# Performance work log

Hardware: AMD Instinct MI355X
Metric: run time of the kernel (lower is better)

Reference implementation:

```python
import jax, jax.numpy as jnp
import numpy as np

N_NODES = 100000
N_EDGES = 1200000
NODE_DIM = 128
HIDDEN = 64
N_POSTS = 50000


def setup_inputs() -> dict:
    key = jax.random.key(0)
    ks = jax.random.split(key, 10)
    s = 1.0 / np.sqrt(NODE_DIM)
    sh = 1.0 / np.sqrt(HIDDEN)
    return {
        "node_features": jax.random.normal(ks[0], (N_NODES, NODE_DIM), dtype=jnp.float32),
        "edge_index": jax.random.randint(ks[1], (2, N_EDGES), 0, N_NODES, dtype=jnp.int64) if jax.config.jax_enable_x64 else jax.random.randint(ks[1], (2, N_EDGES), 0, N_NODES, dtype=jnp.int32),
        "post_mask": jax.random.randint(ks[2], (N_POSTS,), 0, N_NODES, dtype=jnp.int32),
        "W_enc": jax.random.uniform(ks[3], (NODE_DIM, HIDDEN), jnp.float32, -s, s),
        "b_enc": jax.random.uniform(ks[4], (HIDDEN,), jnp.float32, -s, s),
        "W_conv": jax.random.uniform(ks[5], (HIDDEN, HIDDEN), jnp.float32, -sh, sh),
        "b_conv": jax.random.uniform(ks[6], (HIDDEN,), jnp.float32, -sh, sh),
        "W_out": jax.random.uniform(ks[7], (HIDDEN, 1), jnp.float32, -sh, sh),
        "b_out": jax.random.uniform(ks[8], (1,), jnp.float32, -sh, sh),
    }


def reference(node_features, edge_index, post_mask, W_enc, b_enc, W_conv, b_conv, W_out, b_out):
    # encode: relu(Linear)
    node_emb = jax.nn.relu(node_features @ W_enc + b_enc)  # [N, H]
    src, dst = edge_index[0], edge_index[1]
    # per-edge gather then scatter-add into destination nodes (segment sum)
    messages = jax.ops.segment_sum(node_emb[src], dst, num_segments=node_emb.shape[0])  # [N, H]
    node_emb = jax.nn.relu((node_emb + messages) @ W_conv + b_conv)  # [N, H]
    post_emb = node_emb[post_mask]  # [P, H]
    out = jax.nn.sigmoid((post_emb @ W_out + b_out).squeeze(-1))  # [P]
    return out
```

## Files before the change

kernel.cpp:

```cpp
#include <hip/hip_runtime.h>
#include <hip/hip_bf16.h>
#include <math.h>


#define HIDDEN 64
#define NODE_DIM 128
#define SCAN_CHUNK 1024

typedef __attribute__((ext_vector_type(8))) short short8;
typedef __attribute__((ext_vector_type(4))) float floatx4;

union F2B { short8 s; __hip_bfloat162 h[4]; };
union B2U { __hip_bfloat16 b; unsigned short u; };

__device__ inline short8 cvt8(const float4& p, const float4& q) {
    F2B u;
    u.h[0] = __float22bfloat162_rn(make_float2(p.x, p.y));
    u.h[1] = __float22bfloat162_rn(make_float2(p.z, p.w));
    u.h[2] = __float22bfloat162_rn(make_float2(q.x, q.y));
    u.h[3] = __float22bfloat162_rn(make_float2(q.z, q.w));
    return u.s;
}

__device__ inline void cvt8_split(const float4& p, const float4& q,
                                  short8& hi, short8& lo) {
    const float f[8] = {p.x, p.y, p.z, p.w, q.x, q.y, q.z, q.w};
    F2B uh, ul;
    #pragma unroll
    for (int jj = 0; jj < 4; ++jj) {
        const float2 v = make_float2(f[2 * jj], f[2 * jj + 1]);
        const __hip_bfloat162 h = __float22bfloat162_rn(v);
        const float2 hv = __bfloat1622float2(h);
        ul.h[jj] = __float22bfloat162_rn(make_float2(v.x - hv.x, v.y - hv.y));
        uh.h[jj] = h;
    }
    hi = uh.s; lo = ul.s;
}

__global__ __launch_bounds__(256) void k_pre(
    const int* __restrict__ post, unsigned int* __restrict__ bits,
    int* __restrict__ nodelist, int* __restrict__ listCnt,
    int* __restrict__ count, int n_posts, int n_nodes)
{
    const int gtid = blockIdx.x * 256 + threadIdx.x;
    if (gtid < n_nodes) count[gtid] = 0;
    if (gtid < n_posts) {
        const int n = post[gtid];
        const unsigned int bit = 1u << (n & 31);
        const unsigned int old = atomicOr(&bits[n >> 5], bit);
        if (!(old & bit)) {
            const int i = atomicAdd(listCnt, 1);
            nodelist[i] = n;
        }
    }
}

__global__ __launch_bounds__(256) void k_encode_count(
    const float* __restrict__ A, const float* __restrict__ We,
    const float* __restrict__ be, __hip_bfloat16* __restrict__ emb16,
    const int* __restrict__ dsts, const unsigned int* __restrict__ bits,
    int* __restrict__ count, int* __restrict__ rank,
    int n_nodes, int n_tiles, int n_edges)
{
    __shared__ unsigned short sW16[NODE_DIM * HIDDEN];

    {
        const float4* src = (const float4*)We;
        #pragma unroll
        for (int i = 0; i < 8; ++i) {
            const int fidx = i * 256 + threadIdx.x;
            const float4 v = src[fidx];
            #pragma unroll
            for (int c = 0; c < 4; ++c) {
                const int linear = fidx * 4 + c;
                const int k   = linear >> 6;
                const int col = linear & 63;
                const int ks   = k >> 5;
                const int kw   = k & 31;
                const int quad = kw >> 3;
                const int jj   = (kw & 7) >> 1;
                const int b    = kw & 1;
                const int nt   = col >> 4;
                const int r    = col & 15;
                const int dst = ((((ks * 4 + nt) * 4 + quad) * 16 + r) * 8) + jj * 2 + b;
                const float fv = (c == 0) ? v.x : (c == 1) ? v.y : (c == 2) ? v.z : v.w;
                B2U cv; cv.b = __float2bfloat16(fv);
                sW16[dst] = cv.u;
            }
        }
    }
    __syncthreads();

    const int lane = threadIdx.x & 63;
    const int r    = lane & 15;
    const int quad = lane >> 4;

    short8 Wb[4][4];
    #pragma unroll
    for (int ks = 0; ks < 4; ++ks)
        #pragma unroll
        for (int nt = 0; nt < 4; ++nt)
            Wb[ks][nt] = *(const short8*)&sW16[(((ks * 4 + nt) * 4 + quad) * 16 + r) * 8];

    float bias[4];
    #pragma unroll
    for (int nt = 0; nt < 4; ++nt) bias[nt] = be[nt * 16 + r];

    const int wid    = (blockIdx.x * 256 + threadIdx.x) >> 6;
    const int nwaves = gridDim.x * 4;

    const int estride = gridDim.x * 256;
    int e = blockIdx.x * 256 + threadIdx.x;

    for (int t = wid; t < n_tiles; t += nwaves) {
        const float* Arow = A + (size_t)t * 16 * NODE_DIM + (size_t)r * NODE_DIM + quad * 8;
        float4 a[4][2];
        #pragma unroll
        for (int ks = 0; ks < 4; ++ks) {
            a[ks][0] = *(const float4*)(Arow + ks * 32);
            a[ks][1] = *(const float4*)(Arow + ks * 32 + 4);
        }

        #pragma unroll
        for (int q = 0; q < 3; ++q) {
            if (e < n_edges) {
                const int d = dsts[e];
                if ((bits[d >> 5] >> (d & 31)) & 1u)
                    rank[e] = atomicAdd(&count[d], 1);
                e += estride;
            }
        }

        floatx4 acc[4] = {};
        #pragma unroll
        for (int ks = 0; ks < 4; ++ks) {
            const short8 af = cvt8(a[ks][0], a[ks][1]);
            #pragma unroll
            for (int nt = 0; nt < 4; ++nt)
                acc[nt] = __builtin_amdgcn_mfma_f32_16x16x32_bf16(af, Wb[ks][nt], acc[nt], 0, 0, 0);
        }
        #pragma unroll
        for (int nt = 0; nt < 4; ++nt)
            #pragma unroll
            for (int g = 0; g < 4; ++g) {
                const int node = t * 16 + quad * 4 + g;
                const float h = fmaxf(acc[nt][g] + bias[nt], 0.0f);
                emb16[(size_t)node * HIDDEN + nt * 16 + r] = __float2bfloat16(h);
            }
    }
    const int rem = n_nodes - n_tiles * 16;
    if (rem > 0 && wid == 0) {
        for (int n = n_tiles * 16; n < n_nodes; ++n) {
            float acc = be[lane];
            const float* row = A + (size_t)n * NODE_DIM;
            for (int k = 0; k < NODE_DIM; ++k)
                acc = fmaf(row[k], We[(size_t)k * HIDDEN + lane], acc);
            emb16[(size_t)n * HIDDEN + lane] = __float2bfloat16(fmaxf(acc, 0.0f));
        }
    }

    for (; e < n_edges; e += estride) {
        const int d = dsts[e];
        if ((bits[d >> 5] >> (d & 31)) & 1u)
            rank[e] = atomicAdd(&count[d], 1);
    }
}

__global__ __launch_bounds__(256) void k_scan_lb(
    const int* __restrict__ count, int* __restrict__ row_start,
    unsigned int* __restrict__ partials, int n)
{
    __shared__ int s[256];
    __shared__ int sExc;
    const int b = blockIdx.x, tid = threadIdx.x;
    const int base = b * SCAN_CHUNK + tid * 4;
    int c0 = (base + 0 < n) ? count[base + 0] : 0;
    int c1 = (base + 1 < n) ? count[base + 1] : 0;
    int c2 = (base + 2 < n) ? count[base + 2] : 0;
    int c3 = (base + 3 < n) ? count[base + 3] : 0;
    const int t = c0 + c1 + c2 + c3;
    s[tid] = t;
    __syncthreads();
    #pragma unroll
    for (int off = 1; off < 256; off <<= 1) {
        int v = (tid >= off) ? s[tid - off] : 0;
        __syncthreads();
        s[tid] += v;
        __syncthreads();
    }
    const int total = s[255];

    if (b == 0) {
        if (tid == 0) {
            __hip_atomic_store(&partials[0], (2u << 30) | (unsigned int)total,
                               __ATOMIC_RELEASE, __HIP_MEMORY_SCOPE_AGENT);
            sExc = 0;
        }
    } else {
        if (tid == 0) {
            __hip_atomic_store(&partials[b], (1u << 30) | (unsigned int)total,
                               __ATOMIC_RELEASE, __HIP_MEMORY_SCOPE_AGENT);
        }
        if (tid < 64) {
            int exc = 0;
            int winEnd = b;
            while (true) {
                const int j = winEnd - 64 + tid;
                const unsigned int v = (j >= 0)
                    ? __hip_atomic_load(&partials[j], __ATOMIC_ACQUIRE,
                                        __HIP_MEMORY_SCOPE_AGENT)
                    : (2u << 30);
                const unsigned int st = v >> 30;
                if (__ballot(st == 0u)) {
                    __builtin_amdgcn_s_sleep(1);
                    continue;
                }
                const unsigned long long b2 = __ballot(st == 2u);
                int contrib;
                bool done;
                if (b2) {
                    const int hi = 63 - __clzll(b2);
                    contrib = (tid >= hi) ? (int)(v & 0x3FFFFFFFu) : 0;
                    done = true;
                } else {
                    contrib = (int)(v & 0x3FFFFFFFu);
                    done = false;
                }
                #pragma unroll
                for (int off = 1; off < 64; off <<= 1)
                    contrib += __shfl_xor(contrib, off);
                exc += contrib;
                if (done) break;
                winEnd -= 64;
            }
            if (tid == 0) {
                __hip_atomic_store(&partials[b],
                                   (2u << 30) | (unsigned int)(exc + total),
                                   __ATOMIC_RELEASE, __HIP_MEMORY_SCOPE_AGENT);
                sExc = exc;
            }
        }
    }
    __syncthreads();
    int run = sExc + s[tid] - t;
    if (base + 0 < n) row_start[base + 0] = run;           run += c0;
    if (base + 1 < n) row_start[base + 1] = run;           run += c1;
    if (base + 2 < n) row_start[base + 2] = run;           run += c2;
    if (base + 3 < n) row_start[base + 3] = run;
}

__global__ __launch_bounds__(256) void k_fill(
    const int* __restrict__ srcs, const int* __restrict__ dsts,
    const unsigned int* __restrict__ bits, const int* __restrict__ row_start,
    const int* __restrict__ rank, int* __restrict__ slots, int n_edges)
{
    const int stride = gridDim.x * 256;
    for (int e = blockIdx.x * 256 + threadIdx.x; e < n_edges; e += stride) {
        const int d = dsts[e];
        if (!((bits[d >> 5] >> (d & 31)) & 1u)) continue;
        slots[row_start[d] + rank[e]] = srcs[e];
    }
}

__global__ __launch_bounds__(256) void k_gather(
    const int* __restrict__ nodelist, const int* __restrict__ listCnt,
    const int* __restrict__ row_start, const int* __restrict__ count,
    const int* __restrict__ slots, const __hip_bfloat16* __restrict__ emb16,
    float* __restrict__ msg_c)
{
    const int lane = threadIdx.x & 63;
    const int j    = lane & 7;
    const int g    = lane >> 3;
    const int wavei = (blockIdx.x * 256 + threadIdx.x) >> 6;
    const int ngroups = gridDim.x * 4 * 8;
    const int nc   = listCnt[0];

    for (int i = wavei * 8 + g; i < nc; i += ngroups) {
        const int n    = nodelist[i];
        const int m    = count[n];
        const int base = row_start[n];

        float2 a0 = {0.f, 0.f}, a1 = {0.f, 0.f}, a2 = {0.f, 0.f}, a3 = {0.f, 0.f};
        #define ACC8(v)  do { F2B u; u.s = (v); float2 t;                       \
            t = __bfloat1622float2(u.h[0]); a0.x += t.x; a0.y += t.y;           \
            t = __bfloat1622float2(u.h[1]); a1.x += t.x; a1.y += t.y;           \
            t = __bfloat1622float2(u.h[2]); a2.x += t.x; a2.y += t.y;           \
            t = __bfloat1622float2(u.h[3]); a3.x += t.x; a3.y += t.y; } while (0)

        {
            const short8 v = *(const short8*)(emb16 + (size_t)n * HIDDEN + j * 8);
            ACC8(v);
        }
        int c = 0;
        for (; c + 1 < m; c += 2) {
            const int s0 = slots[base + c];
            const int s1 = slots[base + c + 1];
            const short8 v0 = *(const short8*)(emb16 + (size_t)s0 * HIDDEN + j * 8);
            const short8 v1 = *(const short8*)(emb16 + (size_t)s1 * HIDDEN + j * 8);
            ACC8(v0); ACC8(v1);
        }
        if (c < m) {
            const int s0 = slots[base + c];
            const short8 v0 = *(const short8*)(emb16 + (size_t)s0 * HIDDEN + j * 8);
            ACC8(v0);
        }
        #undef ACC8

        float4* dst = (float4*)(msg_c + (size_t)i * HIDDEN + j * 8);
        dst[0] = make_float4(a0.x, a0.y, a1.x, a1.y);
        dst[1] = make_float4(a2.x, a2.y, a3.x, a3.y);
    }
}

__global__ __launch_bounds__(256) void k_head_mfma(
    const int* __restrict__ listCnt, const int* __restrict__ nodelist,
    const float* __restrict__ msg_c,
    const float* __restrict__ Wc, const float* __restrict__ bc,
    const float* __restrict__ Wo, const float* __restrict__ bo,
    float* __restrict__ res)
{
    const int lane = threadIdx.x & 63;
    const int r    = lane & 15;
    const int quad = lane >> 4;

    short8 Wb[2][4];
    #pragma unroll
    for (int ks = 0; ks < 2; ++ks)
        #pragma unroll
        for (int nt = 0; nt < 4; ++nt) {
            F2B u;
            #pragma unroll
            for (int jj = 0; jj < 4; ++jj) {
                const int k0 = ks * 32 + quad * 8 + 2 * jj;
                const float lo = Wc[(size_t)k0 * HIDDEN + nt * 16 + r];
                const float hi = Wc[(size_t)(k0 + 1) * HIDDEN + nt * 16 + r];
                u.h[jj] = __float22bfloat162_rn(make_float2(lo, hi));
            }
            Wb[ks][nt] = u.s;
        }
    float bias[4], wo[4];
    #pragma unroll
    for (int nt = 0; nt < 4; ++nt) { bias[nt] = bc[nt * 16 + r]; wo[nt] = Wo[nt * 16 + r]; }
    const float bo_s = bo[0];

    const int nc      = listCnt[0];
    const int n_tiles = (nc + 15) / 16;
    const int wid     = (blockIdx.x * 256 + threadIdx.x) >> 6;
    const int nwaves  = gridDim.x * 4;

    for (int tile = wid; tile < n_tiles; tile += nwaves) {
        const int i0  = tile * 16;
        const int row = i0 + r;
        floatx4 acc[4] = {};
        #pragma unroll
        for (int ks = 0; ks < 2; ++ks) {
            float4 f0 = make_float4(0.f, 0.f, 0.f, 0.f), f1 = f0;
            if (row < nc) {
                const float* src = msg_c + (size_t)row * HIDDEN + ks * 32 + quad * 8;
                f0 = *(const float4*)src;
                f1 = *(const float4*)(src + 4);
            }
            short8 ah, al;
            cvt8_split(f0, f1, ah, al);
            #pragma unroll
            for (int nt = 0; nt < 4; ++nt) {
                acc[nt] = __builtin_amdgcn_mfma_f32_16x16x32_bf16(ah, Wb[ks][nt], acc[nt], 0, 0, 0);
                acc[nt] = __builtin_amdgcn_mfma_f32_16x16x32_bf16(al, Wb[ks][nt], acc[nt], 0, 0, 0);
            }
        }
        float r4[4];
        #pragma unroll
        for (int gg = 0; gg < 4; ++gg) {
            float part = 0.0f;
            #pragma unroll
            for (int nt = 0; nt < 4; ++nt)
                part += fmaxf(acc[nt][gg] + bias[nt], 0.0f) * wo[nt];
            part += __shfl_xor(part, 1);
            part += __shfl_xor(part, 2);
            part += __shfl_xor(part, 4);
            part += __shfl_xor(part, 8);
            r4[gg] = part;
        }
        if (r == 0) {
            #pragma unroll
            for (int gg = 0; gg < 4; ++gg) {
                const int idx = i0 + quad * 4 + gg;
                if (idx < nc)
                    res[nodelist[idx]] = 1.0f / (1.0f + __expf(-(r4[gg] + bo_s)));
            }
        }
    }
}

__global__ __launch_bounds__(256) void k_out(
    const int* __restrict__ post, const float* __restrict__ res,
    float* __restrict__ out, int n_posts)
{
    const int p = blockIdx.x * 256 + threadIdx.x;
    if (p < n_posts) out[p] = res[post[p]];
}

extern "C" void kernel_launch(void* const* d_in, const int* in_sizes, int n_in,
                              void* d_out, int out_size, void* d_ws, size_t ws_size,
                              hipStream_t stream) {
    const float* A    = (const float*)d_in[0];
    const int*   ei   = (const int*)  d_in[1];
    const int*   post = (const int*)  d_in[2];
    const float* We   = (const float*)d_in[3];
    const float* be   = (const float*)d_in[4];
    const float* Wc   = (const float*)d_in[5];
    const float* bc   = (const float*)d_in[6];
    const float* Wo   = (const float*)d_in[7];
    const float* bo   = (const float*)d_in[8];
    float* out = (float*)d_out;

    const int n_nodes = in_sizes[0] / NODE_DIM;
    const int n_edges = in_sizes[1] / 2;
    const int n_posts = in_sizes[2];

    char* p = (char*)d_ws;
    __hip_bfloat16* emb16 = (__hip_bfloat16*)p;  p += (size_t)n_nodes * HIDDEN * 2;
    float* msg_c    = (float*)p;              p += (size_t)n_posts * HIDDEN * 4;
    int*   slots    = (int*)p;                p += (size_t)n_edges * 4;
    int*   rank     = (int*)p;                p += (size_t)n_edges * 4;
    char* zbase = p;
    unsigned int* bits = (unsigned int*)p;    p += ((size_t)(n_nodes + 31) / 32 + 32) * 4;
    int*   listCnt  = (int*)p;                p += 256;
    unsigned int* partials = (unsigned int*)p; p += 1024;
    const size_t zbytes = (size_t)(p - zbase);
    int*   count    = (int*)p;                p += (size_t)n_nodes * 4;
    int*   row_start= (int*)p;                p += (size_t)n_nodes * 4;
    int*   nodelist = (int*)p;                p += (size_t)n_nodes * 4;
    float* res      = (float*)p;              p += (size_t)n_nodes * 4;

    const int* srcs = ei;
    const int* dsts = ei + n_edges;
    const int nb = (n_nodes + SCAN_CHUNK - 1) / SCAN_CHUNK;
    const int n_tiles = n_nodes / 16;

    (void)hipMemsetAsync(zbase, 0, zbytes, stream);
    k_pre<<<(n_nodes + 255) / 256, 256, 0, stream>>>(post, bits, nodelist, listCnt, count, n_posts, n_nodes);
    k_encode_count<<<1536, 256, 0, stream>>>(A, We, be, emb16, dsts, bits, count, rank, n_nodes, n_tiles, n_edges);
    k_scan_lb<<<nb, 256, 0, stream>>>(count, row_start, partials, n_nodes);
    k_fill<<<2048, 256, 0, stream>>>(srcs, dsts, bits, row_start, rank, slots, n_edges);
    k_gather<<<2048, 256, 0, stream>>>(nodelist, listCnt, row_start, count, slots, emb16, msg_c);
    k_head_mfma<<<1024, 256, 0, stream>>>(listCnt, nodelist, msg_c, Wc, bc, Wo, bo, res);
    k_out<<<(n_posts + 255) / 256, 256, 0, stream>>>(post, res, out, n_posts);
}
```

Measured before the change: 185.7 us.

## Fuse all pipeline stages into one cooperative persistent kernel with grid syncs

```diff
diff --git a/kernel.cpp b/kernel.cpp
--- a/kernel.cpp
+++ b/kernel.cpp
@@ -1,6 +1,9 @@
 #include <hip/hip_runtime.h>
+#include <hip/hip_cooperative_groups.h>
 #include <hip/hip_bf16.h>
 #include <math.h>
+
+namespace cg = cooperative_groups;
 
 
 #define HIDDEN 64
@@ -35,6 +38,349 @@
         uh.h[jj] = h;
     }
     hi = uh.s; lo = ul.s;
+}
+
+__global__ __launch_bounds__(256) void k_mega(
+    const float* __restrict__ A, const int* __restrict__ srcs,
+    const int* __restrict__ dsts, const int* __restrict__ post,
+    const float* __restrict__ We, const float* __restrict__ be,
+    const float* __restrict__ Wc, const float* __restrict__ bc,
+    const float* __restrict__ Wo, const float* __restrict__ bo,
+    float* __restrict__ out,
+    unsigned int* __restrict__ bits, int* __restrict__ nodelist,
+    int* __restrict__ listCnt, unsigned int* __restrict__ partials,
+    int* __restrict__ count, int* __restrict__ row_start,
+    int* __restrict__ rank, int* __restrict__ slots,
+    __hip_bfloat16* __restrict__ emb16, float* __restrict__ msg_c,
+    float* __restrict__ res,
+    int n_nodes, int n_edges, int n_posts, int n_tiles, int nb)
+{
+    cg::grid_group grid = cg::this_grid();
+    __shared__ unsigned short sW16[NODE_DIM * HIDDEN];
+    __shared__ int sS[256];
+    __shared__ int sExc;
+
+    const int tid     = threadIdx.x;
+    const int gstride = gridDim.x * 256;
+    const int gtid0   = blockIdx.x * 256 + tid;
+
+    for (int i = gtid0; i < n_nodes; i += gstride) count[i] = 0;
+    for (int p = gtid0; p < n_posts; p += gstride) {
+        const int n = post[p];
+        const unsigned int bit = 1u << (n & 31);
+        const unsigned int old = atomicOr(&bits[n >> 5], bit);
+        if (!(old & bit)) {
+            const int i = atomicAdd(listCnt, 1);
+            nodelist[i] = n;
+        }
+    }
+    grid.sync();
+
+    {
+        const float4* src = (const float4*)We;
+        #pragma unroll
+        for (int i = 0; i < 8; ++i) {
+            const int fidx = i * 256 + tid;
+            const float4 v = src[fidx];
+            #pragma unroll
+            for (int c = 0; c < 4; ++c) {
+                const int linear = fidx * 4 + c;
+                const int k   = linear >> 6;
+                const int col = linear & 63;
+                const int ks   = k >> 5;
+                const int kw   = k & 31;
+                const int quad = kw >> 3;
+                const int jj   = (kw & 7) >> 1;
+                const int b    = kw & 1;
+                const int nt   = col >> 4;
+                const int r    = col & 15;
+                const int dsti = ((((ks * 4 + nt) * 4 + quad) * 16 + r) * 8) + jj * 2 + b;
+                const float fv = (c == 0) ? v.x : (c == 1) ? v.y : (c == 2) ? v.z : v.w;
+                B2U cv; cv.b = __float2bfloat16(fv);
+                sW16[dsti] = cv.u;
+            }
+        }
+        __syncthreads();
+
+        const int lane = tid & 63;
+        const int r    = lane & 15;
+        const int quad = lane >> 4;
+
+        short8 Wb[4][4];
+        #pragma unroll
+        for (int ks = 0; ks < 4; ++ks)
+            #pragma unroll
+            for (int nt = 0; nt < 4; ++nt)
+                Wb[ks][nt] = *(const short8*)&sW16[(((ks * 4 + nt) * 4 + quad) * 16 + r) * 8];
+
+        float bias[4];
+        #pragma unroll
+        for (int nt = 0; nt < 4; ++nt) bias[nt] = be[nt * 16 + r];
+
+        const int wid    = gtid0 >> 6;
+        const int nwaves = gridDim.x * 4;
+        int e = gtid0;
+
+        for (int t = wid; t < n_tiles; t += nwaves) {
+            const float* Arow = A + (size_t)t * 16 * NODE_DIM + (size_t)r * NODE_DIM + quad * 8;
+            float4 a[4][2];
+            #pragma unroll
+            for (int ks = 0; ks < 4; ++ks) {
+                a[ks][0] = *(const float4*)(Arow + ks * 32);
+                a[ks][1] = *(const float4*)(Arow + ks * 32 + 4);
+            }
+            #pragma unroll
+            for (int q = 0; q < 3; ++q) {
+                if (e < n_edges) {
+                    const int d = dsts[e];
+                    if ((bits[d >> 5] >> (d & 31)) & 1u)
+                        rank[e] = atomicAdd(&count[d], 1);
+                    e += gstride;
+                }
+            }
+            floatx4 acc[4] = {};
+            #pragma unroll
+            for (int ks = 0; ks < 4; ++ks) {
+                const short8 af = cvt8(a[ks][0], a[ks][1]);
+                #pragma unroll
+                for (int nt = 0; nt < 4; ++nt)
+                    acc[nt] = __builtin_amdgcn_mfma_f32_16x16x32_bf16(af, Wb[ks][nt], acc[nt], 0, 0, 0);
+            }
+            #pragma unroll
+            for (int nt = 0; nt < 4; ++nt)
+                #pragma unroll
+                for (int g = 0; g < 4; ++g) {
+                    const int node = t * 16 + quad * 4 + g;
+                    const float h = fmaxf(acc[nt][g] + bias[nt], 0.0f);
+                    emb16[(size_t)node * HIDDEN + nt * 16 + r] = __float2bfloat16(h);
+                }
+        }
+        const int rem = n_nodes - n_tiles * 16;
+        if (rem > 0 && (gtid0 >> 6) == 0) {
+            for (int n = n_tiles * 16; n < n_nodes; ++n) {
+                float accs = be[lane];
+                const float* row = A + (size_t)n * NODE_DIM;
+                for (int k = 0; k < NODE_DIM; ++k)
+                    accs = fmaf(row[k], We[(size_t)k * HIDDEN + lane], accs);
+                emb16[(size_t)n * HIDDEN + lane] = __float2bfloat16(fmaxf(accs, 0.0f));
+            }
+        }
+        for (; e < n_edges; e += gstride) {
+            const int d = dsts[e];
+            if ((bits[d >> 5] >> (d & 31)) & 1u)
+                rank[e] = atomicAdd(&count[d], 1);
+        }
+    }
+    grid.sync();
+
+    if (blockIdx.x < (unsigned)nb) {
+        const int b = blockIdx.x;
+        const int base = b * SCAN_CHUNK + tid * 4;
+        int c0 = (base + 0 < n_nodes) ? count[base + 0] : 0;
+        int c1 = (base + 1 < n_nodes) ? count[base + 1] : 0;
+        int c2 = (base + 2 < n_nodes) ? count[base + 2] : 0;
+        int c3 = (base + 3 < n_nodes) ? count[base + 3] : 0;
+        const int t = c0 + c1 + c2 + c3;
+        sS[tid] = t;
+        __syncthreads();
+        #pragma unroll
+        for (int off = 1; off < 256; off <<= 1) {
+            int v = (tid >= off) ? sS[tid - off] : 0;
+            __syncthreads();
+            sS[tid] += v;
+            __syncthreads();
+        }
+        const int total = sS[255];
+
+        if (b == 0) {
+            if (tid == 0) {
+                __hip_atomic_store(&partials[0], (2u << 30) | (unsigned int)total,
+                                   __ATOMIC_RELEASE, __HIP_MEMORY_SCOPE_AGENT);
+                sExc = 0;
+            }
+        } else {
+            if (tid == 0) {
+                __hip_atomic_store(&partials[b], (1u << 30) | (unsigned int)total,
+                                   __ATOMIC_RELEASE, __HIP_MEMORY_SCOPE_AGENT);
+            }
+            if (tid < 64) {
+                int exc = 0;
+                int winEnd = b;
+                while (true) {
+                    const int j = winEnd - 64 + tid;
+                    const unsigned int v = (j >= 0)
+                        ? __hip_atomic_load(&partials[j], __ATOMIC_ACQUIRE,
+                                            __HIP_MEMORY_SCOPE_AGENT)
+                        : (2u << 30);
+                    const unsigned int st = v >> 30;
+                    if (__ballot(st == 0u)) {
+                        __builtin_amdgcn_s_sleep(1);
+                        continue;
+                    }
+                    const unsigned long long b2 = __ballot(st == 2u);
+                    int contrib;
+                    bool done;
+                    if (b2) {
+                        const int hi = 63 - __clzll(b2);
+                        contrib = (tid >= hi) ? (int)(v & 0x3FFFFFFFu) : 0;
+                        done = true;
+                    } else {
+                        contrib = (int)(v & 0x3FFFFFFFu);
+                        done = false;
+                    }
+                    #pragma unroll
+                    for (int off = 1; off < 64; off <<= 1)
+                        contrib += __shfl_xor(contrib, off);
+                    exc += contrib;
+                    if (done) break;
+                    winEnd -= 64;
+                }
+                if (tid == 0) {
+                    __hip_atomic_store(&partials[b],
+                                       (2u << 30) | (unsigned int)(exc + total),
+                                       __ATOMIC_RELEASE, __HIP_MEMORY_SCOPE_AGENT);
+                    sExc = exc;
+                }
+            }
+        }
+        __syncthreads();
+        int run = sExc + sS[tid] - t;
+        if (base + 0 < n_nodes) row_start[base + 0] = run;   run += c0;
+        if (base + 1 < n_nodes) row_start[base + 1] = run;   run += c1;
+        if (base + 2 < n_nodes) row_start[base + 2] = run;   run += c2;
+        if (base + 3 < n_nodes) row_start[base + 3] = run;
+    }
+    grid.sync();
+
+    for (int e = gtid0; e < n_edges; e += gstride) {
+        const int d = dsts[e];
+        if (!((bits[d >> 5] >> (d & 31)) & 1u)) continue;
+        slots[row_start[d] + rank[e]] = srcs[e];
+    }
+    grid.sync();
+
+    {
+        const int lane = tid & 63;
+        const int j    = lane & 7;
+        const int g    = lane >> 3;
+        const int wavei = gtid0 >> 6;
+        const int ngroups = gridDim.x * 4 * 8;
+        const int nc   = listCnt[0];
+
+        for (int i = wavei * 8 + g; i < nc; i += ngroups) {
+            const int n    = nodelist[i];
+            const int m    = count[n];
+            const int base = row_start[n];
+
+            float2 a0 = {0.f, 0.f}, a1 = {0.f, 0.f}, a2 = {0.f, 0.f}, a3 = {0.f, 0.f};
+            #define ACC8(v)  do { F2B u; u.s = (v); float2 t2;                      \
+                t2 = __bfloat1622float2(u.h[0]); a0.x += t2.x; a0.y += t2.y;        \
+                t2 = __bfloat1622float2(u.h[1]); a1.x += t2.x; a1.y += t2.y;        \
+                t2 = __bfloat1622float2(u.h[2]); a2.x += t2.x; a2.y += t2.y;        \
+                t2 = __bfloat1622float2(u.h[3]); a3.x += t2.x; a3.y += t2.y; } while (0)
+
+            {
+                const short8 v = *(const short8*)(emb16 + (size_t)n * HIDDEN + j * 8);
+                ACC8(v);
+            }
+            int c = 0;
+            for (; c + 1 < m; c += 2) {
+                const int s0 = slots[base + c];
+                const int s1 = slots[base + c + 1];
+                const short8 v0 = *(const short8*)(emb16 + (size_t)s0 * HIDDEN + j * 8);
+                const short8 v1 = *(const short8*)(emb16 + (size_t)s1 * HIDDEN + j * 8);
+                ACC8(v0); ACC8(v1);
+            }
+            if (c < m) {
+                const int s0 = slots[base + c];
+                const short8 v0 = *(const short8*)(emb16 + (size_t)s0 * HIDDEN + j * 8);
+                ACC8(v0);
+            }
+            #undef ACC8
+
+            float4* dst = (float4*)(msg_c + (size_t)i * HIDDEN + j * 8);
+            dst[0] = make_float4(a0.x, a0.y, a1.x, a1.y);
+            dst[1] = make_float4(a2.x, a2.y, a3.x, a3.y);
+        }
+    }
+    grid.sync();
+
+    {
+        const int lane = tid & 63;
+        const int r    = lane & 15;
+        const int quad = lane >> 4;
+
+        short8 Wb[2][4];
+        #pragma unroll
+        for (int ks = 0; ks < 2; ++ks)
+            #pragma unroll
+            for (int nt = 0; nt < 4; ++nt) {
+                F2B u;
+                #pragma unroll
+                for (int jj = 0; jj < 4; ++jj) {
+                    const int k0 = ks * 32 + quad * 8 + 2 * jj;
+                    const float lo = Wc[(size_t)k0 * HIDDEN + nt * 16 + r];
+                    const float hi = Wc[(size_t)(k0 + 1) * HIDDEN + nt * 16 + r];
+                    u.h[jj] = __float22bfloat162_rn(make_float2(lo, hi));
+                }
+                Wb[ks][nt] = u.s;
+            }
+        float bias[4], wo[4];
+        #pragma unroll
+        for (int nt = 0; nt < 4; ++nt) { bias[nt] = bc[nt * 16 + r]; wo[nt] = Wo[nt * 16 + r]; }
+        const float bo_s = bo[0];
+
+        const int nc      = listCnt[0];
+        const int nt_h    = (nc + 15) / 16;
+        const int wid     = gtid0 >> 6;
+        const int nwaves  = gridDim.x * 4;
+
+        for (int tile = wid; tile < nt_h; tile += nwaves) {
+            const int i0  = tile * 16;
+            const int row = i0 + r;
+            floatx4 acc[4] = {};
+            #pragma unroll
+            for (int ks = 0; ks < 2; ++ks) {
+                float4 f0 = make_float4(0.f, 0.f, 0.f, 0.f), f1 = f0;
+                if (row < nc) {
+                    const float* src2 = msg_c + (size_t)row * HIDDEN + ks * 32 + quad * 8;
+                    f0 = *(const float4*)src2;
+                    f1 = *(const float4*)(src2 + 4);
+                }
+                short8 ah, al;
+                cvt8_split(f0, f1, ah, al);
+                #pragma unroll
+                for (int nt = 0; nt < 4; ++nt) {
+                    acc[nt] = __builtin_amdgcn_mfma_f32_16x16x32_bf16(ah, Wb[ks][nt], acc[nt], 0, 0, 0);
+                    acc[nt] = __builtin_amdgcn_mfma_f32_16x16x32_bf16(al, Wb[ks][nt], acc[nt], 0, 0, 0);
+                }
+            }
+            float r4[4];
+            #pragma unroll
+            for (int gg = 0; gg < 4; ++gg) {
+                float part = 0.0f;
+                #pragma unroll
+                for (int nt = 0; nt < 4; ++nt)
+                    part += fmaxf(acc[nt][gg] + bias[nt], 0.0f) * wo[nt];
+                part += __shfl_xor(part, 1);
+                part += __shfl_xor(part, 2);
+                part += __shfl_xor(part, 4);
+                part += __shfl_xor(part, 8);
+                r4[gg] = part;
+            }
+            if (r == 0) {
+                #pragma unroll
+                for (int gg = 0; gg < 4; ++gg) {
+                    const int idx = i0 + quad * 4 + gg;
+                    if (idx < nc)
+                        res[nodelist[idx]] = 1.0f / (1.0f + __expf(-(r4[gg] + bo_s)));
+                }
+            }
+        }
+    }
+    grid.sync();
+
+    for (int p = gtid0; p < n_posts; p += gstride) out[p] = res[post[p]];
 }
 
 __global__ __launch_bounds__(256) void k_pre(
@@ -63,7 +409,6 @@
     int n_nodes, int n_tiles, int n_edges)
 {
     __shared__ unsigned short sW16[NODE_DIM * HIDDEN];
-
     {
         const float4* src = (const float4*)We;
         #pragma unroll
@@ -108,7 +453,6 @@
 
     const int wid    = (blockIdx.x * 256 + threadIdx.x) >> 6;
     const int nwaves = gridDim.x * 4;
-
     const int estride = gridDim.x * 256;
     int e = blockIdx.x * 256 + threadIdx.x;
 
@@ -120,7 +464,6 @@
             a[ks][0] = *(const float4*)(Arow + ks * 32);
             a[ks][1] = *(const float4*)(Arow + ks * 32 + 4);
         }
-
         #pragma unroll
         for (int q = 0; q < 3; ++q) {
             if (e < n_edges) {
@@ -130,7 +473,6 @@
                 e += estride;
             }
         }
-
         floatx4 acc[4] = {};
         #pragma unroll
         for (int ks = 0; ks < 4; ++ks) {
@@ -158,7 +500,6 @@
             emb16[(size_t)n * HIDDEN + lane] = __float2bfloat16(fmaxf(acc, 0.0f));
         }
     }
-
     for (; e < n_edges; e += estride) {
         const int d = dsts[e];
         if ((bits[d >> 5] >> (d & 31)) & 1u)
@@ -414,9 +755,9 @@
     const float* bo   = (const float*)d_in[8];
     float* out = (float*)d_out;
 
-    const int n_nodes = in_sizes[0] / NODE_DIM;
-    const int n_edges = in_sizes[1] / 2;
-    const int n_posts = in_sizes[2];
+    int n_nodes = in_sizes[0] / NODE_DIM;
+    int n_edges = in_sizes[1] / 2;
+    int n_posts = in_sizes[2];
 
     char* p = (char*)d_ws;
     __hip_bfloat16* emb16 = (__hip_bfloat16*)p;  p += (size_t)n_nodes * HIDDEN * 2;
@@ -435,15 +776,42 @@
 
     const int* srcs = ei;
     const int* dsts = ei + n_edges;
-    const int nb = (n_nodes + SCAN_CHUNK - 1) / SCAN_CHUNK;
-    const int n_tiles = n_nodes / 16;
+    int nb = (n_nodes + SCAN_CHUNK - 1) / SCAN_CHUNK;
+    int n_tiles = n_nodes / 16;
+
+    static int s_grid = 0;
+    if (s_grid == 0) {
+        hipDeviceProp_t prop;
+        if (hipGetDeviceProperties(&prop, 0) != hipSuccess) prop.multiProcessorCount = 256;
+        int maxB = 0;
+        if (hipOccupancyMaxActiveBlocksPerMultiprocessor(&maxB, k_mega, 256, 0) != hipSuccess || maxB < 1)
+            maxB = 1;
+        long g = (long)maxB * prop.multiProcessorCount;
+        if (g > 2048) g = 2048;
+        if (g < 256)  g = 256;
+        s_grid = (int)g;
+    }
 
     (void)hipMemsetAsync(zbase, 0, zbytes, stream);
-    k_pre<<<(n_nodes + 255) / 256, 256, 0, stream>>>(post, bits, nodelist, listCnt, count, n_posts, n_nodes);
-    k_encode_count<<<1536, 256, 0, stream>>>(A, We, be, emb16, dsts, bits, count, rank, n_nodes, n_tiles, n_edges);
-    k_scan_lb<<<nb, 256, 0, stream>>>(count, row_start, partials, n_nodes);
-    k_fill<<<2048, 256, 0, stream>>>(srcs, dsts, bits, row_start, rank, slots, n_edges);
-    k_gather<<<2048, 256, 0, stream>>>(nodelist, listCnt, row_start, count, slots, emb16, msg_c);
-    k_head_mfma<<<1024, 256, 0, stream>>>(listCnt, nodelist, msg_c, Wc, bc, Wo, bo, res);
-    k_out<<<(n_posts + 255) / 256, 256, 0, stream>>>(post, res, out, n_posts);
-}
+
+    void* args[] = {
+        (void*)&A, (void*)&srcs, (void*)&dsts, (void*)&post,
+        (void*)&We, (void*)&be, (void*)&Wc, (void*)&bc, (void*)&Wo, (void*)&bo,
+        (void*)&out,
+        (void*)&bits, (void*)&nodelist, (void*)&listCnt, (void*)&partials,
+        (void*)&count, (void*)&row_start, (void*)&rank, (void*)&slots,
+        (void*)&emb16, (void*)&msg_c, (void*)&res,
+        (void*)&n_nodes, (void*)&n_edges, (void*)&n_posts, (void*)&n_tiles, (void*)&nb
+    };
+    hipError_t err = hipLaunchCooperativeKernel((const void*)k_mega, dim3(s_grid), dim3(256),
+                                                args, 0, stream);
+    if (err != hipSuccess) {
+        k_pre<<<(n_nodes + 255) / 256, 256, 0, stream>>>(post, bits, nodelist, listCnt, count, n_posts, n_nodes);
+        k_encode_count<<<1536, 256, 0, stream>>>(A, We, be, emb16, dsts, bits, count, rank, n_nodes, n_tiles, n_edges);
+        k_scan_lb<<<nb, 256, 0, stream>>>(count, row_start, partials, n_nodes);
+        k_fill<<<2048, 256, 0, stream>>>(srcs, dsts, bits, row_start, rank, slots, n_edges);
+        k_gather<<<2048, 256, 0, stream>>>(nodelist, listCnt, row_start, count, slots, emb16, msg_c);
+        k_head_mfma<<<1024, 256, 0, stream>>>(listCnt, nodelist, msg_c, Wc, bc, Wo, bo, res);
+        k_out<<<(n_posts + 255) / 256, 256, 0, stream>>>(post, res, out, n_posts);
+    }
+}
```

After: 403.2 us. +117.1%, slower.

## Fuse neighbor gather into MFMA head kernel, dropping msg_c buffer

Applied to the files above, without the earlier changes.

```diff
diff --git a/kernel.cpp b/kernel.cpp
--- a/kernel.cpp
+++ b/kernel.cpp
@@ -262,59 +262,10 @@
     }
 }
 
-__global__ __launch_bounds__(256) void k_gather(
+__global__ __launch_bounds__(256) void k_gather_head(
     const int* __restrict__ nodelist, const int* __restrict__ listCnt,
     const int* __restrict__ row_start, const int* __restrict__ count,
     const int* __restrict__ slots, const __hip_bfloat16* __restrict__ emb16,
-    float* __restrict__ msg_c)
-{
-    const int lane = threadIdx.x & 63;
-    const int j    = lane & 7;
-    const int g    = lane >> 3;
-    const int wavei = (blockIdx.x * 256 + threadIdx.x) >> 6;
-    const int ngroups = gridDim.x * 4 * 8;
-    const int nc   = listCnt[0];
-
-    for (int i = wavei * 8 + g; i < nc; i += ngroups) {
-        const int n    = nodelist[i];
-        const int m    = count[n];
-        const int base = row_start[n];
-
-        float2 a0 = {0.f, 0.f}, a1 = {0.f, 0.f}, a2 = {0.f, 0.f}, a3 = {0.f, 0.f};
-        #define ACC8(v)  do { F2B u; u.s = (v); float2 t;                       \
-            t = __bfloat1622float2(u.h[0]); a0.x += t.x; a0.y += t.y;           \
-            t = __bfloat1622float2(u.h[1]); a1.x += t.x; a1.y += t.y;           \
-            t = __bfloat1622float2(u.h[2]); a2.x += t.x; a2.y += t.y;           \
-            t = __bfloat1622float2(u.h[3]); a3.x += t.x; a3.y += t.y; } while (0)
-
-        {
-            const short8 v = *(const short8*)(emb16 + (size_t)n * HIDDEN + j * 8);
-            ACC8(v);
-        }
-        int c = 0;
-        for (; c + 1 < m; c += 2) {
-            const int s0 = slots[base + c];
-            const int s1 = slots[base + c + 1];
-            const short8 v0 = *(const short8*)(emb16 + (size_t)s0 * HIDDEN + j * 8);
-            const short8 v1 = *(const short8*)(emb16 + (size_t)s1 * HIDDEN + j * 8);
-            ACC8(v0); ACC8(v1);
-        }
-        if (c < m) {
-            const int s0 = slots[base + c];
-            const short8 v0 = *(const short8*)(emb16 + (size_t)s0 * HIDDEN + j * 8);
-            ACC8(v0);
-        }
-        #undef ACC8
-
-        float4* dst = (float4*)(msg_c + (size_t)i * HIDDEN + j * 8);
-        dst[0] = make_float4(a0.x, a0.y, a1.x, a1.y);
-        dst[1] = make_float4(a2.x, a2.y, a3.x, a3.y);
-    }
-}
-
-__global__ __launch_bounds__(256) void k_head_mfma(
-    const int* __restrict__ listCnt, const int* __restrict__ nodelist,
-    const float* __restrict__ msg_c,
     const float* __restrict__ Wc, const float* __restrict__ bc,
     const float* __restrict__ Wo, const float* __restrict__ bo,
     float* __restrict__ res)
@@ -351,21 +302,69 @@
     for (int tile = wid; tile < n_tiles; tile += nwaves) {
         const int i0  = tile * 16;
         const int row = i0 + r;
+
+        float4 f0a = make_float4(0.f, 0.f, 0.f, 0.f), f0b = f0a;
+        float4 f1a = f0a, f1b = f0a;
+        if (row < nc) {
+            const int n    = nodelist[row];
+            const int m    = count[n];
+            const int base = row_start[n];
+            const size_t o0 = (size_t)n * HIDDEN + quad * 8;
+
+            #define ACC2(vlo, vhi) do {                                          \
+                F2B ua, ub; ua.s = (vlo); ub.s = (vhi); float2 t2;               \
+                t2 = __bfloat1622float2(ua.h[0]); f0a.x += t2.x; f0a.y += t2.y;  \
+                t2 = __bfloat1622float2(ua.h[1]); f0a.z += t2.x; f0a.w += t2.y;  \
+                t2 = __bfloat1622float2(ua.h[2]); f0b.x += t2.x; f0b.y += t2.y;  \
+                t2 = __bfloat1622float2(ua.h[3]); f0b.z += t2.x; f0b.w += t2.y;  \
+                t2 = __bfloat1622float2(ub.h[0]); f1a.x += t2.x; f1a.y += t2.y;  \
+                t2 = __bfloat1622float2(ub.h[1]); f1a.z += t2.x; f1a.w += t2.y;  \
+                t2 = __bfloat1622float2(ub.h[2]); f1b.x += t2.x; f1b.y += t2.y;  \
+                t2 = __bfloat1622float2(ub.h[3]); f1b.z += t2.x; f1b.w += t2.y;  \
+            } while (0)
+
+            {
+                const short8 vlo = *(const short8*)(emb16 + o0);
+                const short8 vhi = *(const short8*)(emb16 + o0 + 32);
+                ACC2(vlo, vhi);
+            }
+            int c = 0;
+            for (; c + 1 < m; c += 2) {
+                const int s0 = slots[base + c];
+                const int s1 = slots[base + c + 1];
+                const size_t a0 = (size_t)s0 * HIDDEN + quad * 8;
+                const size_t a1 = (size_t)s1 * HIDDEN + quad * 8;
+                const short8 v0lo = *(const short8*)(emb16 + a0);
+                const short8 v0hi = *(const short8*)(emb16 + a0 + 32);
+                const short8 v1lo = *(const short8*)(emb16 + a1);
+                const short8 v1hi = *(const short8*)(emb16 + a1 + 32);
+                ACC2(v0lo, v0hi);
+                ACC2(v1lo, v1hi);
+            }
+            if (c < m) {
+                const int s0 = slots[base + c];
+                const size_t a0 = (size_t)s0 * HIDDEN + quad * 8;
+                const short8 v0lo = *(const short8*)(emb16 + a0);
+                const short8 v0hi = *(const short8*)(emb16 + a0 + 32);
+                ACC2(v0lo, v0hi);
+            }
+            #undef ACC2
+        }
+
         floatx4 acc[4] = {};
-        #pragma unroll
-        for (int ks = 0; ks < 2; ++ks) {
-            float4 f0 = make_float4(0.f, 0.f, 0.f, 0.f), f1 = f0;
-            if (row < nc) {
-                const float* src = msg_c + (size_t)row * HIDDEN + ks * 32 + quad * 8;
-                f0 = *(const float4*)src;
-                f1 = *(const float4*)(src + 4);
-            }
+        {
             short8 ah, al;
-            cvt8_split(f0, f1, ah, al);
+            cvt8_split(f0a, f0b, ah, al);
             #pragma unroll
             for (int nt = 0; nt < 4; ++nt) {
-                acc[nt] = __builtin_amdgcn_mfma_f32_16x16x32_bf16(ah, Wb[ks][nt], acc[nt], 0, 0, 0);
-                acc[nt] = __builtin_amdgcn_mfma_f32_16x16x32_bf16(al, Wb[ks][nt], acc[nt], 0, 0, 0);
+                acc[nt] = __builtin_amdgcn_mfma_f32_16x16x32_bf16(ah, Wb[0][nt], acc[nt], 0, 0, 0);
+                acc[nt] = __builtin_amdgcn_mfma_f32_16x16x32_bf16(al, Wb[0][nt], acc[nt], 0, 0, 0);
+            }
+            cvt8_split(f1a, f1b, ah, al);
+            #pragma unroll
+            for (int nt = 0; nt < 4; ++nt) {
+                acc[nt] = __builtin_amdgcn_mfma_f32_16x16x32_bf16(ah, Wb[1][nt], acc[nt], 0, 0, 0);
+                acc[nt] = __builtin_amdgcn_mfma_f32_16x16x32_bf16(al, Wb[1][nt], acc[nt], 0, 0, 0);
             }
         }
         float r4[4];
@@ -420,7 +419,6 @@
 
     char* p = (char*)d_ws;
     __hip_bfloat16* emb16 = (__hip_bfloat16*)p;  p += (size_t)n_nodes * HIDDEN * 2;
-    float* msg_c    = (float*)p;              p += (size_t)n_posts * HIDDEN * 4;
     int*   slots    = (int*)p;                p += (size_t)n_edges * 4;
     int*   rank     = (int*)p;                p += (size_t)n_edges * 4;
     char* zbase = p;
@@ -443,7 +441,6 @@
     k_encode_count<<<1536, 256, 0, stream>>>(A, We, be, emb16, dsts, bits, count, rank, n_nodes, n_tiles, n_edges);
     k_scan_lb<<<nb, 256, 0, stream>>>(count, row_start, partials, n_nodes);
     k_fill<<<2048, 256, 0, stream>>>(srcs, dsts, bits, row_start, rank, slots, n_edges);
-    k_gather<<<2048, 256, 0, stream>>>(nodelist, listCnt, row_start, count, slots, emb16, msg_c);
-    k_head_mfma<<<1024, 256, 0, stream>>>(listCnt, nodelist, msg_c, Wc, bc, Wo, bo, res);
+    k_gather_head<<<1024, 256, 0, stream>>>(nodelist, listCnt, row_start, count, slots, emb16, Wc, bc, Wo, bo, res);
     k_out<<<(n_posts + 255) / 256, 256, 0, stream>>>(post, res, out, n_posts);
 }
```

New measurement: 181.9 us. 1.02x faster.
